# Kernel tuning notes

Hardware: AMD Instinct MI355X
Metric: run time of the kernel (lower is better)

The kernel has to match this reference:

```python
import jax, jax.numpy as jnp
import numpy as np

B, NPG, D_IN, D, L = 64, 512, 1, 128, 10
N = B * NPG
DEG = 16
E = N * DEG
EPS = 1e-5


def setup_inputs() -> dict:
    key = jax.random.key(0)
    ks = jax.random.split(key, 8)
    x = jax.random.normal(ks[0], (N, D_IN), jnp.float32)
    # edges confined within each graph: local indices + per-graph offset
    src_local = jax.random.randint(ks[1], (E,), 0, NPG)
    dst_local = jax.random.randint(ks[2], (E,), 0, NPG)
    offs = (jnp.arange(E) // (E // B)) * NPG
    edge_src = (src_local + offs).astype(jnp.int32)
    edge_dst = (dst_local + offs).astype(jnp.int32)
    batch = jnp.repeat(jnp.arange(B, dtype=jnp.int32), NPG)
    g = lambda k, s, fan: jax.random.normal(k, s, jnp.float32) / np.float32(np.sqrt(fan))
    W0 = g(ks[3], (D_IN, D), D_IN)
    b0 = jnp.zeros((D,), jnp.float32)
    W_rest = g(ks[4], (L - 1, D, D), D)
    b_rest = jnp.zeros((L - 1, D), jnp.float32)
    gamma = jnp.ones((L, D), jnp.float32)
    beta = jnp.zeros((L, D), jnp.float32)
    W_att = g(ks[5], (D, D), D)
    return dict(x=x, edge_src=edge_src, edge_dst=edge_dst, batch=batch,
                W0=W0, b0=b0, W_rest=W_rest, b_rest=b_rest,
                gamma=gamma, beta=beta, W_att=W_att)


def _gcn_conv(h, W, b, src, dst, norm_e, self_w):
    # GCNConv: h' = D^-1/2 (A + I) D^-1/2 (h W) + b  (symmetric norm, self-loops)
    h = h @ W
    msg = norm_e[:, None] * h[src]                      # [E, D] gather
    agg = jax.ops.segment_sum(msg, dst, num_segments=N)  # [N, D] scatter-add
    return agg + self_w[:, None] * h + b


def _bn_relu(h, g, b):
    mu = jnp.mean(h, axis=0)
    var = jnp.var(h, axis=0)
    return jax.nn.relu(g * (h - mu) * jax.lax.rsqrt(var + EPS) + b)


def reference(x, edge_src, edge_dst, batch, W0, b0, W_rest, b_rest, gamma, beta, W_att):
    # symmetric GCN normalization with self-loops (edge weight 1)
    deg = 1.0 + jax.ops.segment_sum(jnp.ones((E,), x.dtype), edge_dst, num_segments=N)
    dinv = jax.lax.rsqrt(deg)
    norm_e = dinv[edge_src] * dinv[edge_dst]   # [E]
    self_w = dinv * dinv                        # [N] self-loop coefficient

    h = _gcn_conv(x, W0, b0, edge_src, edge_dst, norm_e, self_w)
    h = _bn_relu(h, gamma[0], beta[0])
    for l in range(L - 1):
        h = _gcn_conv(h, W_rest[l], b_rest[l], edge_src, edge_dst, norm_e, self_w)
        h = _bn_relu(h, gamma[l + 1], beta[l + 1])

    # graph attention pooling
    mean = jax.ops.segment_sum(h, batch, num_segments=B) / jnp.float32(NPG)  # [B, D]
    tg = jnp.tanh(mean @ W_att)                                              # [B, D]
    coefs = jax.nn.sigmoid(jnp.sum(h * tg[batch], axis=1) * 10.0)            # [N]
    graph_feat = jax.ops.segment_sum(coefs[:, None] * h, batch, num_segments=B)  # [B, D]

    # to_dense_batch (equal-sized graphs -> exact reshape) + concat broadcast graph feat
    node_dense = h.reshape(B, NPG, D)
    gf = jnp.broadcast_to(graph_feat[:, None, :], (B, NPG, D))
    return jnp.concatenate([node_dense, gf], axis=-1)  # [B, NPG, 2D]
```

## Files before the change

kernel.cpp:

```cpp
#include <hip/hip_runtime.h>
#include <hip/hip_bf16.h>
#include <math.h>

#define NN 32768
#define BG 64
#define NPGC 512
#define DD 128
#define EE 524288
#define LL 10
#define EPSF 1e-5f
#define PADK 72

typedef __attribute__((ext_vector_type(8))) short short8;
typedef __attribute__((ext_vector_type(4))) float float4v;

static __device__ __forceinline__ unsigned short f2bf(float x) {
    __hip_bfloat16 b = __float2bfloat16(x);
    return *reinterpret_cast<unsigned short*>(&b);
}
static __device__ __forceinline__ float bf2f(unsigned short u) {
    unsigned int v = ((unsigned int)u) << 16;
    return __uint_as_float(v);
}
static __device__ __forceinline__ void splitbf(float x, unsigned short& h, unsigned short& l) {
    unsigned short hh = f2bf(x);
    h = hh;
    l = f2bf(x - bf2f(hh));
}


__global__ void k_histM(const int* __restrict__ src, const int* __restrict__ dst,
                        unsigned int* __restrict__ Mp, int* __restrict__ cnt) {
    int e = blockIdx.x * 256 + threadIdx.x;
    int d = dst[e], s = src[e] & 511;
    int cell = (d << 9) + s;
    atomicAdd(&Mp[cell >> 1], 1u << ((cell & 1) << 4));
    atomicAdd(&cnt[d], 1);
}

__global__ void k_dinv(const int* __restrict__ cnt, float* __restrict__ dinv) {
    int n = blockIdx.x * 256 + threadIdx.x;
    dinv[n] = rsqrtf(1.0f + (float)cnt[n]);
}

__global__ void k_conv(const unsigned int* __restrict__ Mp, unsigned short* __restrict__ Mh) {
    int idx = (blockIdx.x * 256 + threadIdx.x) * 8;
    uint4 v = *(const uint4*)(Mp + (idx >> 1));
    unsigned int c[8] = {v.x & 0xffffu, v.x >> 16, v.y & 0xffffu, v.y >> 16,
                         v.z & 0xffffu, v.z >> 16, v.w & 0xffffu, v.w >> 16};
    int diag = (idx >> 9) & 511;
    int cb = idx & 511;
    unsigned short us[8];
    #pragma unroll
    for (int j = 0; j < 8; j++)
        us[j] = f2bf((float)(c[j] + ((cb + j == diag) ? 1u : 0u)));
    *(uint4*)(Mh + idx) = *(uint4*)us;
}

__global__ void k_wt(const float* __restrict__ Wr, unsigned short* __restrict__ Wt_h,
                     unsigned short* __restrict__ Wt_l) {
    int idx = blockIdx.x * 256 + threadIdx.x;
    int l = idx >> 14, rem = idx & 16383;
    int fp = rem >> 7, f = rem & 127;
    unsigned short h, lo;
    splitbf(Wr[l * 16384 + f * 128 + fp], h, lo);
    Wt_h[idx] = h;
    Wt_l[idx] = lo;
}

__global__ void k_l0(const float* __restrict__ x, const float* __restrict__ W0,
                     const float* __restrict__ dinv,
                     unsigned short* __restrict__ hwT_h, unsigned short* __restrict__ hwT_l) {
    int u = blockIdx.x * 256 + threadIdx.x;
    int f = u >> 12, n0 = (u & 4095) * 8;
    float w = W0[f];
    float4 xa = *(const float4*)(x + n0);
    float4 xb = *(const float4*)(x + n0 + 4);
    float4 da = *(const float4*)(dinv + n0);
    float4 db = *(const float4*)(dinv + n0 + 4);
    float v[8] = {xa.x * w * da.x, xa.y * w * da.y, xa.z * w * da.z, xa.w * w * da.w,
                  xb.x * w * db.x, xb.y * w * db.y, xb.z * w * db.z, xb.w * w * db.w};
    unsigned short uh[8], ul[8];
    #pragma unroll
    for (int i = 0; i < 8; i++) splitbf(v[i], uh[i], ul[i]);
    *(uint4*)(hwT_h + (size_t)f * NN + n0) = *(uint4*)uh;
    *(uint4*)(hwT_l + (size_t)f * NN + n0) = *(uint4*)ul;
}

__global__ __launch_bounds__(256) void k_aggmm(const unsigned short* __restrict__ Mh,
        const unsigned short* __restrict__ hwT_h, const unsigned short* __restrict__ hwT_l,
        const float* __restrict__ dinv, const float* __restrict__ bias,
        float* __restrict__ pre, float* __restrict__ stats) {
    __shared__ unsigned short As[128 * PADK];
    __shared__ unsigned short Bs_h[128 * PADK], Bs_l[128 * PADK];
    int t = threadIdx.x, lane = t & 63, wv = t >> 6;
    int l15 = lane & 15, quad = lane >> 4;
    int b = blockIdx.x, r = b & 7, q = b >> 3;
    int g = r + 8 * (q & 7);
    int mb = (q >> 3) * 128;
    size_t arow = ((size_t)g * 512 + mb) * 512;
    size_t gcol = (size_t)g * 512;
    float4v acc[16];
    #pragma unroll
    for (int i = 0; i < 16; i++) acc[i] = (float4v)0.f;

    for (int kc = 0; kc < 512; kc += 64) {
        __syncthreads();
        #pragma unroll
        for (int i = 0; i < 4; i++) {
            int u = t + i * 256;
            int row = u >> 3, ko = (u & 7) * 8;
            *(uint4*)(&As[row * PADK + ko]) =
                *(const uint4*)(Mh + arow + (size_t)row * 512 + kc + ko);
        }
        #pragma unroll
        for (int i = 0; i < 4; i++) {
            int u = t + i * 256;
            int f = u >> 3, ko = (u & 7) * 8;
            size_t go = (size_t)f * NN + gcol + kc + ko;
            *(uint4*)(&Bs_h[f * PADK + ko]) = *(const uint4*)(hwT_h + go);
            *(uint4*)(&Bs_l[f * PADK + ko]) = *(const uint4*)(hwT_l + go);
        }
        __syncthreads();
        int f0 = wv * 32;
        #pragma unroll
        for (int ks = 0; ks < 2; ks++) {
            int kb = ks * 32 + quad * 8;
            short8 a[8];
            #pragma unroll
            for (int mt = 0; mt < 8; mt++)
                a[mt] = *(const short8*)(&As[(mt * 16 + l15) * PADK + kb]);
            #pragma unroll
            for (int nt = 0; nt < 2; nt++) {
                short8 bh = *(const short8*)(&Bs_h[(f0 + nt * 16 + l15) * PADK + kb]);
                short8 bl = *(const short8*)(&Bs_l[(f0 + nt * 16 + l15) * PADK + kb]);
                #pragma unroll
                for (int mt = 0; mt < 8; mt++) {
                    acc[mt * 2 + nt] = __builtin_amdgcn_mfma_f32_16x16x32_bf16(a[mt], bh, acc[mt * 2 + nt], 0, 0, 0);
                    acc[mt * 2 + nt] = __builtin_amdgcn_mfma_f32_16x16x32_bf16(a[mt], bl, acc[mt * 2 + nt], 0, 0, 0);
                }
            }
        }
    }
    int gbase = g * 512 + mb;
    int fA = wv * 32 + l15;
    float bf0 = bias[fA], bf1 = bias[fA + 16];
    float cs[2] = {0.f, 0.f}, cq[2] = {0.f, 0.f};
    #pragma unroll
    for (int mt = 0; mt < 8; mt++) {
        int n0 = gbase + mt * 16 + quad * 4;
        float4 dv = *(const float4*)(dinv + n0);
        #pragma unroll
        for (int nt = 0; nt < 2; nt++) {
            int f = fA + nt * 16;
            float bf = nt ? bf1 : bf0;
            float4v a = acc[mt * 2 + nt];
            float v0 = fmaf(dv.x, a[0], bf);
            float v1 = fmaf(dv.y, a[1], bf);
            float v2 = fmaf(dv.z, a[2], bf);
            float v3 = fmaf(dv.w, a[3], bf);
            pre[(size_t)(n0 + 0) * 128 + f] = v0;
            pre[(size_t)(n0 + 1) * 128 + f] = v1;
            pre[(size_t)(n0 + 2) * 128 + f] = v2;
            pre[(size_t)(n0 + 3) * 128 + f] = v3;
            cs[nt] += v0 + v1 + v2 + v3;
            cq[nt] = fmaf(v0, v0, cq[nt]); cq[nt] = fmaf(v1, v1, cq[nt]);
            cq[nt] = fmaf(v2, v2, cq[nt]); cq[nt] = fmaf(v3, v3, cq[nt]);
        }
    }
    #pragma unroll
    for (int nt = 0; nt < 2; nt++) {
        float cs_ = cs[nt], cq_ = cq[nt];
        cs_ += __shfl_xor(cs_, 16); cs_ += __shfl_xor(cs_, 32);
        cq_ += __shfl_xor(cq_, 16); cq_ += __shfl_xor(cq_, 32);
        if (quad == 0) {
            atomicAdd(&stats[fA + nt * 16], cs_);
            atomicAdd(&stats[128 + fA + nt * 16], cq_);
        }
    }
}

__global__ __launch_bounds__(256) void k_mmT(const float* __restrict__ pre,
        const float* __restrict__ stats, const float* __restrict__ gamma,
        const float* __restrict__ beta, const float* __restrict__ dinv,
        const unsigned short* __restrict__ Wt_h, const unsigned short* __restrict__ Wt_l,
        unsigned short* __restrict__ hwT_h, unsigned short* __restrict__ hwT_l) {
    __shared__ unsigned short Ws_h[128 * PADK], Ws_l[128 * PADK];
    __shared__ unsigned short Xs_h[64 * PADK], Xs_l[64 * PADK];
    __shared__ float scL[256];
    int t = threadIdx.x, lane = t & 63, wv = t >> 6;
    int l15 = lane & 15, quad = lane >> 4;
    int b = blockIdx.x, r = b & 7, q = b >> 3;
    int g = r + 8 * (q & 7);
    int nb = g * NPGC + (q >> 3) * 64;
    if (t < 128) {
        float mu = stats[t] * (1.0f / NN);
        float var = stats[128 + t] * (1.0f / NN) - mu * mu;
        float s = gamma[t] * rsqrtf(var + EPSF);
        scL[t] = s;
        scL[128 + t] = fmaf(-mu, s, beta[t]);
    }
    float4v acc[8];
    #pragma unroll
    for (int i = 0; i < 8; i++) acc[i] = (float4v)0.f;

    for (int kc = 0; kc < 128; kc += 64) {
        __syncthreads();
        #pragma unroll
        for (int i = 0; i < 4; i++) {
            int u = t + i * 256;
            int fp = u >> 3, ko = (u & 7) * 8;
            int go = fp * 128 + kc + ko;
            *(uint4*)(&Ws_h[fp * PADK + ko]) = *(const uint4*)(Wt_h + go);
            *(uint4*)(&Ws_l[fp * PADK + ko]) = *(const uint4*)(Wt_l + go);
        }
        #pragma unroll
        for (int i = 0; i < 2; i++) {
            int u = t + i * 256;
            int n = u >> 3, fo = (u & 7) * 8;
            const float* pp = pre + (size_t)(nb + n) * 128 + kc + fo;
            float4 v0 = *(const float4*)(pp);
            float4 v1 = *(const float4*)(pp + 4);
            float4 s0 = *(const float4*)(&scL[kc + fo]);
            float4 s1 = *(const float4*)(&scL[kc + fo + 4]);
            float4 h0 = *(const float4*)(&scL[128 + kc + fo]);
            float4 h1 = *(const float4*)(&scL[128 + kc + fo + 4]);
            float v[8] = {fmaxf(fmaf(v0.x, s0.x, h0.x), 0.f),
                          fmaxf(fmaf(v0.y, s0.y, h0.y), 0.f),
                          fmaxf(fmaf(v0.z, s0.z, h0.z), 0.f),
                          fmaxf(fmaf(v0.w, s0.w, h0.w), 0.f),
                          fmaxf(fmaf(v1.x, s1.x, h1.x), 0.f),
                          fmaxf(fmaf(v1.y, s1.y, h1.y), 0.f),
                          fmaxf(fmaf(v1.z, s1.z, h1.z), 0.f),
                          fmaxf(fmaf(v1.w, s1.w, h1.w), 0.f)};
            unsigned short uh[8], ul[8];
            #pragma unroll
            for (int j = 0; j < 8; j++) splitbf(v[j], uh[j], ul[j]);
            *(uint4*)(&Xs_h[n * PADK + fo]) = *(uint4*)uh;
            *(uint4*)(&Xs_l[n * PADK + fo]) = *(uint4*)ul;
        }
        __syncthreads();
        int m0 = wv * 32;
        #pragma unroll
        for (int ks = 0; ks < 2; ks++) {
            int kb = ks * 32 + quad * 8;
            short8 a0h = *(const short8*)(&Ws_h[(m0 + l15) * PADK + kb]);
            short8 a0l = *(const short8*)(&Ws_l[(m0 + l15) * PADK + kb]);
            short8 a1h = *(const short8*)(&Ws_h[(m0 + 16 + l15) * PADK + kb]);
            short8 a1l = *(const short8*)(&Ws_l[(m0 + 16 + l15) * PADK + kb]);
            #pragma unroll
            for (int nt = 0; nt < 4; nt++) {
                short8 bh = *(const short8*)(&Xs_h[(nt * 16 + l15) * PADK + kb]);
                short8 bl = *(const short8*)(&Xs_l[(nt * 16 + l15) * PADK + kb]);
                acc[nt]     = __builtin_amdgcn_mfma_f32_16x16x32_bf16(a0h, bh, acc[nt], 0, 0, 0);
                acc[nt]     = __builtin_amdgcn_mfma_f32_16x16x32_bf16(a0h, bl, acc[nt], 0, 0, 0);
                acc[nt]     = __builtin_amdgcn_mfma_f32_16x16x32_bf16(a0l, bh, acc[nt], 0, 0, 0);
                acc[4 + nt] = __builtin_amdgcn_mfma_f32_16x16x32_bf16(a1h, bh, acc[4 + nt], 0, 0, 0);
                acc[4 + nt] = __builtin_amdgcn_mfma_f32_16x16x32_bf16(a1h, bl, acc[4 + nt], 0, 0, 0);
                acc[4 + nt] = __builtin_amdgcn_mfma_f32_16x16x32_bf16(a1l, bh, acc[4 + nt], 0, 0, 0);
            }
        }
    }
    #pragma unroll
    for (int mt = 0; mt < 2; mt++) {
        #pragma unroll
        for (int nt = 0; nt < 4; nt++) {
            int n = nb + nt * 16 + l15;
            float dv = dinv[n];
            int fp0 = wv * 32 + mt * 16 + quad * 4;
            float4v a = acc[mt * 4 + nt];
            #pragma unroll
            for (int rg = 0; rg < 4; rg++) {
                unsigned short h, lo;
                splitbf(dv * a[rg], h, lo);
                hwT_h[(size_t)(fp0 + rg) * NN + n] = h;
                hwT_l[(size_t)(fp0 + rg) * NN + n] = lo;
            }
        }
    }
}

__global__ __launch_bounds__(256) void k_bn_pool(float* __restrict__ pre,
        const float* __restrict__ stats, const float* __restrict__ gamma,
        const float* __restrict__ beta, float* __restrict__ meansum) {
    __shared__ float ssum[256];
    __shared__ float scL[256];
    int t = threadIdx.x;
    int b = blockIdx.x, r = b & 7, q = b >> 3;
    int g = r + 8 * (q & 7);
    int nb = g * NPGC + (q >> 3) * 64;
    if (t < 128) {
        float mu = stats[t] * (1.0f / NN);
        float var = stats[128 + t] * (1.0f / NN) - mu * mu;
        float s = gamma[t] * rsqrtf(var + EPSF);
        scL[t] = s;
        scL[128 + t] = fmaf(-mu, s, beta[t]);
    }
    __syncthreads();
    int f = t & 127;
    float s = scL[f], sh = scL[128 + f];
    float lsum = 0.f;
    int base = nb * 128;
    for (int i = 0; i < 32; i++) {
        int idx = base + i * 256 + t;
        float v = fmaxf(fmaf(pre[idx], s, sh), 0.f);
        pre[idx] = v;
        lsum += v;
    }
    ssum[t] = lsum;
    __syncthreads();
    if (t < 128) atomicAdd(&meansum[g * 128 + f], ssum[t] + ssum[t + 128]);
}

__global__ void k_tg(const float* __restrict__ meansum, const float* __restrict__ Watt,
                     float* __restrict__ tg) {
    __shared__ float m[128];
    int g = blockIdx.x, t = threadIdx.x;
    m[t] = meansum[g * 128 + t] * (1.0f / NPGC);
    __syncthreads();
    float a2 = 0.f;
    for (int k = 0; k < 128; k++) a2 = fmaf(m[k], Watt[k * 128 + t], a2);
    tg[g * 128 + t] = tanhf(a2);
}

__global__ __launch_bounds__(256) void k_coef_gf(const float* __restrict__ h,
        const float* __restrict__ tg, float* __restrict__ gf) {
    __shared__ float tgs[128];
    __shared__ float coef[64];
    int t = threadIdx.x;
    int b = blockIdx.x, r = b & 7, q = b >> 3;
    int g = r + 8 * (q & 7);
    int n0 = (q >> 3) * 64;
    if (t < 128) tgs[t] = tg[g * 128 + t];
    __syncthreads();
    int wid = t >> 6, lane = t & 63;
    const float* hp = h + (size_t)g * NPGC * 128;
    for (int j = wid; j < 64; j += 4) {
        int n = n0 + j;
        float p = hp[n * 128 + lane] * tgs[lane] + hp[n * 128 + 64 + lane] * tgs[64 + lane];
        for (int off = 32; off; off >>= 1) p += __shfl_xor(p, off);
        if (lane == 0) coef[j] = 1.0f / (1.0f + expf(-10.0f * p));
    }
    __syncthreads();
    int f = t & 127, half = t >> 7;
    float acc = 0.f;
    for (int j = 0; j < 32; j++) {
        int jj = half * 32 + j;
        acc = fmaf(coef[jj], hp[(n0 + jj) * 128 + f], acc);
    }
    atomicAdd(&gf[g * 128 + f], acc);
}

__global__ void k_out(const float* __restrict__ h, const float* __restrict__ gf,
                      float* __restrict__ out) {
    int idx = blockIdx.x * 256 + threadIdx.x;
    int c4 = (idx & 63) * 4;
    int n = idx >> 6;
    int g = n >> 9;
    float4 v = (c4 < 128) ? *(const float4*)(h + (size_t)n * 128 + c4)
                          : *(const float4*)(gf + g * 128 + (c4 - 128));
    *(float4*)(out + (size_t)idx * 4) = v;
}

extern "C" void kernel_launch(void* const* d_in, const int* in_sizes, int n_in,
                              void* d_out, int out_size, void* d_ws, size_t ws_size,
                              hipStream_t stream) {
    const float* x     = (const float*)d_in[0];
    const int*   esrc  = (const int*)d_in[1];
    const int*   edst  = (const int*)d_in[2];
    const float* W0    = (const float*)d_in[4];
    const float* b0    = (const float*)d_in[5];
    const float* Wr    = (const float*)d_in[6];
    const float* br    = (const float*)d_in[7];
    const float* gamma = (const float*)d_in[8];
    const float* beta  = (const float*)d_in[9];
    const float* Watt  = (const float*)d_in[10];
    float* out = (float*)d_out;
    float* ws  = (float*)d_ws;

    int*   cnt     = (int*)(ws + 0);
    float* dinv    = ws + 32768;
    float* stats   = ws + 65536;
    float* tgbuf   = ws + 68096;
    float* meansum = ws + 76288;
    float* gf      = ws + 84480;
    unsigned short* Wt_h  = (unsigned short*)(ws + 92672);
    unsigned short* Wt_l  = (unsigned short*)(ws + 166400);
    unsigned short* hwT_h = (unsigned short*)(ws + 240128);
    unsigned short* hwT_l = (unsigned short*)(ws + 2337280);
    unsigned short* Mh    = (unsigned short*)(ws + 4434432);
    unsigned int* Mp = (unsigned int*)(ws + 12823040);
    float* pre     = ws + 12823040;

    hipMemsetAsync(cnt, 0, NN * sizeof(int), stream);
    hipMemsetAsync(stats, 0, LL * 256 * sizeof(float), stream);
    hipMemsetAsync(meansum, 0, BG * 128 * sizeof(float), stream);
    hipMemsetAsync(gf, 0, BG * 128 * sizeof(float), stream);
    hipMemsetAsync(Mp, 0, (size_t)NN * 256 * sizeof(int), stream);

    k_histM<<<EE / 256, 256, 0, stream>>>(esrc, edst, Mp, cnt);
    k_dinv<<<NN / 256, 256, 0, stream>>>(cnt, dinv);
    k_conv<<<NN * 512 / 8 / 256, 256, 0, stream>>>(Mp, Mh);
    k_wt<<<9 * 16384 / 256, 256, 0, stream>>>(Wr, Wt_h, Wt_l);
    k_l0<<<128 * (NN / 8) / 256, 256, 0, stream>>>(x, W0, dinv, hwT_h, hwT_l);

    for (int l = 0; l < LL; l++) {
        const float* bias = (l == 0) ? b0 : br + (l - 1) * DD;
        k_aggmm<<<NN / 128, 256, 0, stream>>>(Mh, hwT_h, hwT_l, dinv, bias,
                                              pre, stats + l * 256);
        if (l < LL - 1)
            k_mmT<<<NN / 64, 256, 0, stream>>>(pre, stats + l * 256, gamma + l * DD,
                                               beta + l * DD, dinv, Wt_h + l * 16384,
                                               Wt_l + l * 16384, hwT_h, hwT_l);
        else
            k_bn_pool<<<NN / 64, 256, 0, stream>>>(pre, stats + l * 256, gamma + l * DD,
                                                   beta + l * DD, meansum);
    }
    k_tg<<<BG, 128, 0, stream>>>(meansum, Watt, tgbuf);
    k_coef_gf<<<NN / 64, 256, 0, stream>>>(pre, tgbuf, gf);
    k_out<<<NN * 64 / 256, 256, 0, stream>>>(pre, gf, out);
}
```

Measured before the change: 520.9 us.

## Halve aggmm row tile and load weights directly into registers in mmT

k_aggmm now processes 64 node rows per block instead of 128 and launches twice as many blocks (512 instead of 256), which gives more parallelism on the 256-CU device at the cost of reloading each graph's hw tile twice as often. k_mmT drops its LDS staging of the weight tile. Each wave now reads its W hi/lo fragments straight from global memory into registers, and the whole 128-wide normalized activation tile is staged in LDS in one pass, so the K loop has no __syncthreads between chunks. This cuts LDS traffic and barriers but raises register pressure.

```diff
diff --git a/kernel.cpp b/kernel.cpp
--- a/kernel.cpp
+++ b/kernel.cpp
@@ -10,6 +10,7 @@
 #define LL 10
 #define EPSF 1e-5f
 #define PADK 72
+#define PADW 136
 
 typedef __attribute__((ext_vector_type(8))) short short8;
 typedef __attribute__((ext_vector_type(4))) float float4v;
@@ -91,27 +92,31 @@
         const unsigned short* __restrict__ hwT_h, const unsigned short* __restrict__ hwT_l,
         const float* __restrict__ dinv, const float* __restrict__ bias,
         float* __restrict__ pre, float* __restrict__ stats) {
-    __shared__ unsigned short As[128 * PADK];
+    __shared__ unsigned short As[64 * PADK];
     __shared__ unsigned short Bs_h[128 * PADK], Bs_l[128 * PADK];
     int t = threadIdx.x, lane = t & 63, wv = t >> 6;
     int l15 = lane & 15, quad = lane >> 4;
     int b = blockIdx.x, r = b & 7, q = b >> 3;
     int g = r + 8 * (q & 7);
-    int mb = (q >> 3) * 128;
+    int mb = (q >> 3) * 64;
     size_t arow = ((size_t)g * 512 + mb) * 512;
     size_t gcol = (size_t)g * 512;
-    float4v acc[16];
-    #pragma unroll
-    for (int i = 0; i < 16; i++) acc[i] = (float4v)0.f;
+    float4v acc[8];
+    #pragma unroll
+    for (int i = 0; i < 8; i++) acc[i] = (float4v)0.f;
 
     for (int kc = 0; kc < 512; kc += 64) {
         __syncthreads();
-        #pragma unroll
-        for (int i = 0; i < 4; i++) {
-            int u = t + i * 256;
-            int row = u >> 3, ko = (u & 7) * 8;
-            *(uint4*)(&As[row * PADK + ko]) =
-                *(const uint4*)(Mh + arow + (size_t)row * 512 + kc + ko);
+        {
+            int i = t >> 7;
+            #pragma unroll
+            for (int it = 0; it < 2; it++) {
+                int u = t + it * 256;
+                int row = u >> 3, ko = (u & 7) * 8;
+                *(uint4*)(&As[row * PADK + ko]) =
+                    *(const uint4*)(Mh + arow + (size_t)row * 512 + kc + ko);
+            }
+            (void)i;
         }
         #pragma unroll
         for (int i = 0; i < 4; i++) {
@@ -126,16 +131,16 @@
         #pragma unroll
         for (int ks = 0; ks < 2; ks++) {
             int kb = ks * 32 + quad * 8;
-            short8 a[8];
+            short8 a[4];
             #pragma unroll
-            for (int mt = 0; mt < 8; mt++)
+            for (int mt = 0; mt < 4; mt++)
                 a[mt] = *(const short8*)(&As[(mt * 16 + l15) * PADK + kb]);
             #pragma unroll
             for (int nt = 0; nt < 2; nt++) {
                 short8 bh = *(const short8*)(&Bs_h[(f0 + nt * 16 + l15) * PADK + kb]);
                 short8 bl = *(const short8*)(&Bs_l[(f0 + nt * 16 + l15) * PADK + kb]);
                 #pragma unroll
-                for (int mt = 0; mt < 8; mt++) {
+                for (int mt = 0; mt < 4; mt++) {
                     acc[mt * 2 + nt] = __builtin_amdgcn_mfma_f32_16x16x32_bf16(a[mt], bh, acc[mt * 2 + nt], 0, 0, 0);
                     acc[mt * 2 + nt] = __builtin_amdgcn_mfma_f32_16x16x32_bf16(a[mt], bl, acc[mt * 2 + nt], 0, 0, 0);
                 }
@@ -147,7 +152,7 @@
     float bf0 = bias[fA], bf1 = bias[fA + 16];
     float cs[2] = {0.f, 0.f}, cq[2] = {0.f, 0.f};
     #pragma unroll
-    for (int mt = 0; mt < 8; mt++) {
+    for (int mt = 0; mt < 4; mt++) {
         int n0 = gbase + mt * 16 + quad * 4;
         float4 dv = *(const float4*)(dinv + n0);
         #pragma unroll
@@ -185,8 +190,7 @@
         const float* __restrict__ beta, const float* __restrict__ dinv,
         const unsigned short* __restrict__ Wt_h, const unsigned short* __restrict__ Wt_l,
         unsigned short* __restrict__ hwT_h, unsigned short* __restrict__ hwT_l) {
-    __shared__ unsigned short Ws_h[128 * PADK], Ws_l[128 * PADK];
-    __shared__ unsigned short Xs_h[64 * PADK], Xs_l[64 * PADK];
+    __shared__ unsigned short Xs_h[64 * PADW], Xs_l[64 * PADW];
     __shared__ float scL[256];
     int t = threadIdx.x, lane = t & 63, wv = t >> 6;
     int l15 = lane & 15, quad = lane >> 4;
@@ -200,64 +204,58 @@
         scL[t] = s;
         scL[128 + t] = fmaf(-mu, s, beta[t]);
     }
+    __syncthreads();
+    #pragma unroll
+    for (int i = 0; i < 4; i++) {
+        int u = t + i * 256;
+        int n = u >> 4, fo = (u & 15) * 8;
+        const float* pp = pre + (size_t)(nb + n) * 128 + fo;
+        float4 v0 = *(const float4*)(pp);
+        float4 v1 = *(const float4*)(pp + 4);
+        float4 s0 = *(const float4*)(&scL[fo]);
+        float4 s1 = *(const float4*)(&scL[fo + 4]);
+        float4 h0 = *(const float4*)(&scL[128 + fo]);
+        float4 h1 = *(const float4*)(&scL[128 + fo + 4]);
+        float v[8] = {fmaxf(fmaf(v0.x, s0.x, h0.x), 0.f),
+                      fmaxf(fmaf(v0.y, s0.y, h0.y), 0.f),
+                      fmaxf(fmaf(v0.z, s0.z, h0.z), 0.f),
+                      fmaxf(fmaf(v0.w, s0.w, h0.w), 0.f),
+                      fmaxf(fmaf(v1.x, s1.x, h1.x), 0.f),
+                      fmaxf(fmaf(v1.y, s1.y, h1.y), 0.f),
+                      fmaxf(fmaf(v1.z, s1.z, h1.z), 0.f),
+                      fmaxf(fmaf(v1.w, s1.w, h1.w), 0.f)};
+        unsigned short uh[8], ul[8];
+        #pragma unroll
+        for (int j = 0; j < 8; j++) splitbf(v[j], uh[j], ul[j]);
+        *(uint4*)(&Xs_h[n * PADW + fo]) = *(uint4*)uh;
+        *(uint4*)(&Xs_l[n * PADW + fo]) = *(uint4*)ul;
+    }
+    __syncthreads();
+    int m0 = wv * 32;
+    short8 wh[2][4], wl[2][4];
+    #pragma unroll
+    for (int mt = 0; mt < 2; mt++)
+        #pragma unroll
+        for (int kt = 0; kt < 4; kt++) {
+            int ad = (m0 + mt * 16 + l15) * 128 + kt * 32 + quad * 8;
+            wh[mt][kt] = *(const short8*)(Wt_h + ad);
+            wl[mt][kt] = *(const short8*)(Wt_l + ad);
+        }
     float4v acc[8];
     #pragma unroll
     for (int i = 0; i < 8; i++) acc[i] = (float4v)0.f;
-
-    for (int kc = 0; kc < 128; kc += 64) {
-        __syncthreads();
-        #pragma unroll
-        for (int i = 0; i < 4; i++) {
-            int u = t + i * 256;
-            int fp = u >> 3, ko = (u & 7) * 8;
-            int go = fp * 128 + kc + ko;
-            *(uint4*)(&Ws_h[fp * PADK + ko]) = *(const uint4*)(Wt_h + go);
-            *(uint4*)(&Ws_l[fp * PADK + ko]) = *(const uint4*)(Wt_l + go);
-        }
-        #pragma unroll
-        for (int i = 0; i < 2; i++) {
-            int u = t + i * 256;
-            int n = u >> 3, fo = (u & 7) * 8;
-            const float* pp = pre + (size_t)(nb + n) * 128 + kc + fo;
-            float4 v0 = *(const float4*)(pp);
-            float4 v1 = *(const float4*)(pp + 4);
-            float4 s0 = *(const float4*)(&scL[kc + fo]);
-            float4 s1 = *(const float4*)(&scL[kc + fo + 4]);
-            float4 h0 = *(const float4*)(&scL[128 + kc + fo]);
-            float4 h1 = *(const float4*)(&scL[128 + kc + fo + 4]);
-            float v[8] = {fmaxf(fmaf(v0.x, s0.x, h0.x), 0.f),
-                          fmaxf(fmaf(v0.y, s0.y, h0.y), 0.f),
-                          fmaxf(fmaf(v0.z, s0.z, h0.z), 0.f),
-                          fmaxf(fmaf(v0.w, s0.w, h0.w), 0.f),
-                          fmaxf(fmaf(v1.x, s1.x, h1.x), 0.f),
-                          fmaxf(fmaf(v1.y, s1.y, h1.y), 0.f),
-                          fmaxf(fmaf(v1.z, s1.z, h1.z), 0.f),
-                          fmaxf(fmaf(v1.w, s1.w, h1.w), 0.f)};
-            unsigned short uh[8], ul[8];
+    #pragma unroll
+    for (int kt = 0; kt < 4; kt++) {
+        int kb = kt * 32 + quad * 8;
+        #pragma unroll
+        for (int nt = 0; nt < 4; nt++) {
+            short8 bh = *(const short8*)(&Xs_h[(nt * 16 + l15) * PADW + kb]);
+            short8 bl = *(const short8*)(&Xs_l[(nt * 16 + l15) * PADW + kb]);
             #pragma unroll
-            for (int j = 0; j < 8; j++) splitbf(v[j], uh[j], ul[j]);
-            *(uint4*)(&Xs_h[n * PADK + fo]) = *(uint4*)uh;
-            *(uint4*)(&Xs_l[n * PADK + fo]) = *(uint4*)ul;
-        }
-        __syncthreads();
-        int m0 = wv * 32;
-        #pragma unroll
-        for (int ks = 0; ks < 2; ks++) {
-            int kb = ks * 32 + quad * 8;
-            short8 a0h = *(const short8*)(&Ws_h[(m0 + l15) * PADK + kb]);
-            short8 a0l = *(const short8*)(&Ws_l[(m0 + l15) * PADK + kb]);
-            short8 a1h = *(const short8*)(&Ws_h[(m0 + 16 + l15) * PADK + kb]);
-            short8 a1l = *(const short8*)(&Ws_l[(m0 + 16 + l15) * PADK + kb]);
-            #pragma unroll
-            for (int nt = 0; nt < 4; nt++) {
-                short8 bh = *(const short8*)(&Xs_h[(nt * 16 + l15) * PADK + kb]);
-                short8 bl = *(const short8*)(&Xs_l[(nt * 16 + l15) * PADK + kb]);
-                acc[nt]     = __builtin_amdgcn_mfma_f32_16x16x32_bf16(a0h, bh, acc[nt], 0, 0, 0);
-                acc[nt]     = __builtin_amdgcn_mfma_f32_16x16x32_bf16(a0h, bl, acc[nt], 0, 0, 0);
-                acc[nt]     = __builtin_amdgcn_mfma_f32_16x16x32_bf16(a0l, bh, acc[nt], 0, 0, 0);
-                acc[4 + nt] = __builtin_amdgcn_mfma_f32_16x16x32_bf16(a1h, bh, acc[4 + nt], 0, 0, 0);
-                acc[4 + nt] = __builtin_amdgcn_mfma_f32_16x16x32_bf16(a1h, bl, acc[4 + nt], 0, 0, 0);
-                acc[4 + nt] = __builtin_amdgcn_mfma_f32_16x16x32_bf16(a1l, bh, acc[4 + nt], 0, 0, 0);
+            for (int mt = 0; mt < 2; mt++) {
+                acc[mt * 4 + nt] = __builtin_amdgcn_mfma_f32_16x16x32_bf16(wh[mt][kt], bh, acc[mt * 4 + nt], 0, 0, 0);
+                acc[mt * 4 + nt] = __builtin_amdgcn_mfma_f32_16x16x32_bf16(wh[mt][kt], bl, acc[mt * 4 + nt], 0, 0, 0);
+                acc[mt * 4 + nt] = __builtin_amdgcn_mfma_f32_16x16x32_bf16(wl[mt][kt], bh, acc[mt * 4 + nt], 0, 0, 0);
             }
         }
     }
@@ -406,8 +404,8 @@
 
     for (int l = 0; l < LL; l++) {
         const float* bias = (l == 0) ? b0 : br + (l - 1) * DD;
-        k_aggmm<<<NN / 128, 256, 0, stream>>>(Mh, hwT_h, hwT_l, dinv, bias,
-                                              pre, stats + l * 256);
+        k_aggmm<<<NN / 64, 256, 0, stream>>>(Mh, hwT_h, hwT_l, dinv, bias,
+                                             pre, stats + l * 256);
         if (l < LL - 1)
             k_mmT<<<NN / 64, 256, 0, stream>>>(pre, stats + l * 256, gamma + l * DD,
                                                beta + l * DD, dinv, Wt_h + l * 16384,
```

Measured after the change: 549.2 us. +5.4%, slower.

## Store dense per-graph adjacency counts as uint8 and convert to bf16 in-kernel

Applied to the files above, without the earlier changes.

The per-graph dense adjacency count matrix is now built directly as 8-bit counts through byte-packed atomics, instead of 16-bit counts that a separate pass converted to a bf16 matrix. The self-loop diagonal is added by a small kernel, and the aggregation GEMM converts uint8 to bf16 while staging tiles into shared memory. This drops the conversion kernel and the large intermediate buffers and halves the adjacency bytes read by each of the ten aggregation launches. The cost is extra ALU work per tile load, and a count saturating past 255 would carry into the neighbouring byte, which is unlikely at this edge density.

```diff
diff --git a/kernel.cpp b/kernel.cpp
--- a/kernel.cpp
+++ b/kernel.cpp
@@ -34,27 +34,18 @@
     int e = blockIdx.x * 256 + threadIdx.x;
     int d = dst[e], s = src[e] & 511;
     int cell = (d << 9) + s;
-    atomicAdd(&Mp[cell >> 1], 1u << ((cell & 1) << 4));
+    atomicAdd(&Mp[cell >> 2], 1u << ((cell & 3) << 3));
     atomicAdd(&cnt[d], 1);
+}
+
+__global__ void k_diag(unsigned char* __restrict__ Mu8) {
+    int n = blockIdx.x * 256 + threadIdx.x;
+    Mu8[(size_t)n * 512 + (n & 511)] += 1;
 }
 
 __global__ void k_dinv(const int* __restrict__ cnt, float* __restrict__ dinv) {
     int n = blockIdx.x * 256 + threadIdx.x;
     dinv[n] = rsqrtf(1.0f + (float)cnt[n]);
-}
-
-__global__ void k_conv(const unsigned int* __restrict__ Mp, unsigned short* __restrict__ Mh) {
-    int idx = (blockIdx.x * 256 + threadIdx.x) * 8;
-    uint4 v = *(const uint4*)(Mp + (idx >> 1));
-    unsigned int c[8] = {v.x & 0xffffu, v.x >> 16, v.y & 0xffffu, v.y >> 16,
-                         v.z & 0xffffu, v.z >> 16, v.w & 0xffffu, v.w >> 16};
-    int diag = (idx >> 9) & 511;
-    int cb = idx & 511;
-    unsigned short us[8];
-    #pragma unroll
-    for (int j = 0; j < 8; j++)
-        us[j] = f2bf((float)(c[j] + ((cb + j == diag) ? 1u : 0u)));
-    *(uint4*)(Mh + idx) = *(uint4*)us;
 }
 
 __global__ void k_wt(const float* __restrict__ Wr, unsigned short* __restrict__ Wt_h,
@@ -87,7 +78,7 @@
     *(uint4*)(hwT_l + (size_t)f * NN + n0) = *(uint4*)ul;
 }
 
-__global__ __launch_bounds__(256) void k_aggmm(const unsigned short* __restrict__ Mh,
+__global__ __launch_bounds__(256) void k_aggmm(const unsigned char* __restrict__ Mu8,
         const unsigned short* __restrict__ hwT_h, const unsigned short* __restrict__ hwT_l,
         const float* __restrict__ dinv, const float* __restrict__ bias,
         float* __restrict__ pre, float* __restrict__ stats) {
@@ -110,8 +101,17 @@
         for (int i = 0; i < 4; i++) {
             int u = t + i * 256;
             int row = u >> 3, ko = (u & 7) * 8;
-            *(uint4*)(&As[row * PADK + ko]) =
-                *(const uint4*)(Mh + arow + (size_t)row * 512 + kc + ko);
+            uint2 w = *(const uint2*)(Mu8 + arow + (size_t)row * 512 + kc + ko);
+            unsigned short us[8];
+            us[0] = f2bf((float)(w.x & 0xffu));
+            us[1] = f2bf((float)((w.x >> 8) & 0xffu));
+            us[2] = f2bf((float)((w.x >> 16) & 0xffu));
+            us[3] = f2bf((float)(w.x >> 24));
+            us[4] = f2bf((float)(w.y & 0xffu));
+            us[5] = f2bf((float)((w.y >> 8) & 0xffu));
+            us[6] = f2bf((float)((w.y >> 16) & 0xffu));
+            us[7] = f2bf((float)(w.y >> 24));
+            *(uint4*)(&As[row * PADK + ko]) = *(uint4*)us;
         }
         #pragma unroll
         for (int i = 0; i < 4; i++) {
@@ -388,25 +388,24 @@
     unsigned short* Wt_l  = (unsigned short*)(ws + 166400);
     unsigned short* hwT_h = (unsigned short*)(ws + 240128);
     unsigned short* hwT_l = (unsigned short*)(ws + 2337280);
-    unsigned short* Mh    = (unsigned short*)(ws + 4434432);
-    unsigned int* Mp = (unsigned int*)(ws + 12823040);
-    float* pre     = ws + 12823040;
+    unsigned char*  Mu8   = (unsigned char*)(ws + 4434432);
+    float* pre     = ws + 8628736;
 
     hipMemsetAsync(cnt, 0, NN * sizeof(int), stream);
     hipMemsetAsync(stats, 0, LL * 256 * sizeof(float), stream);
     hipMemsetAsync(meansum, 0, BG * 128 * sizeof(float), stream);
     hipMemsetAsync(gf, 0, BG * 128 * sizeof(float), stream);
-    hipMemsetAsync(Mp, 0, (size_t)NN * 256 * sizeof(int), stream);
-
-    k_histM<<<EE / 256, 256, 0, stream>>>(esrc, edst, Mp, cnt);
+    hipMemsetAsync(Mu8, 0, (size_t)NN * 512, stream);
+
+    k_histM<<<EE / 256, 256, 0, stream>>>(esrc, edst, (unsigned int*)Mu8, cnt);
+    k_diag<<<NN / 256, 256, 0, stream>>>(Mu8);
     k_dinv<<<NN / 256, 256, 0, stream>>>(cnt, dinv);
-    k_conv<<<NN * 512 / 8 / 256, 256, 0, stream>>>(Mp, Mh);
     k_wt<<<9 * 16384 / 256, 256, 0, stream>>>(Wr, Wt_h, Wt_l);
     k_l0<<<128 * (NN / 8) / 256, 256, 0, stream>>>(x, W0, dinv, hwT_h, hwT_l);
 
     for (int l = 0; l < LL; l++) {
         const float* bias = (l == 0) ? b0 : br + (l - 1) * DD;
-        k_aggmm<<<NN / 128, 256, 0, stream>>>(Mh, hwT_h, hwT_l, dinv, bias,
+        k_aggmm<<<NN / 128, 256, 0, stream>>>(Mu8, hwT_h, hwT_l, dinv, bias,
                                               pre, stats + l * 256);
         if (l < LL - 1)
             k_mmT<<<NN / 64, 256, 0, stream>>>(pre, stats + l * 256, gamma + l * DD,
```

Measured after the change: 500.0 us, median of 2. 4.0% less time.
